# Performance work log

Hardware: AMD Instinct MI355X
Metric: run time of the kernel (lower is better)

The kernel has to match this reference:

```python
import jax, jax.numpy as jnp
import numpy as np

N = 6144          # num utterances (graph nodes)
D = 128           # utt_embed_size
WIN = 10          # att_window_size
NUM_SPK = 8
N_EMO = 7


def _init(key, shape):
    fan_in = shape[0]
    return jax.random.normal(key, shape, dtype=jnp.float32) * (1.0 / np.sqrt(fan_in))


def setup_inputs() -> dict:
    key = jax.random.key(0)
    ks = jax.random.split(key, 20)
    inp = {
        "x": jax.random.normal(ks[0], (N, D), dtype=jnp.float32),
        "speakers": jax.random.randint(ks[1], (N,), 0, NUM_SPK, dtype=jnp.int32),
        # layer-1 relation GCN weights (pred / suc / same / diff)
        "W_pred1": _init(ks[2], (D, D)),
        "W_suc1": _init(ks[3], (D, D)),
        "W_same1": _init(ks[4], (D, D)),
        "W_diff1": _init(ks[5], (D, D)),
        # layer-2 relation GCN weights
        "W_pred2": _init(ks[6], (D, D)),
        "W_suc2": _init(ks[7], (D, D)),
        "W_same2": _init(ks[8], (D, D)),
        "W_diff2": _init(ks[9], (D, D)),
        "w_aggr_1": _init(ks[10], (D, D)),
        "w_aggr_2": _init(ks[11], (D, D)),
        "w_e1": _init(ks[12], (2 * D, D)),
        "b_e1": jnp.zeros((D,), dtype=jnp.float32),
        "w_e2": _init(ks[13], (D, N_EMO)),
        "b_e2": jnp.zeros((N_EMO,), dtype=jnp.float32),
        "w_s": _init(ks[14], (2 * D, N_EMO)),
        "b_s": jnp.zeros((N_EMO,), dtype=jnp.float32),
    }
    return inp


def reference(x, speakers, W_pred1, W_suc1, W_same1, W_diff1,
              W_pred2, W_suc2, W_same2, W_diff2,
              w_aggr_1, w_aggr_2, w_e1, b_e1, w_e2, b_e2, w_s, b_s):
    n = x.shape[0]
    idx = jnp.arange(n)
    # windowed dot-product attention; entries outside the window stay 0.0
    # BEFORE the softmax (faithful to the torch code: zeros, not -inf)
    band = jnp.abs(idx[:, None] - idx[None, :]) <= WIN
    scores = jnp.where(band, x @ x.T, 0.0)            # [N, N]
    attn = jax.nn.softmax(scores, axis=1)
    # relation masks
    same = (speakers[:, None] == speakers[None, :]).astype(x.dtype)
    pred = (idx[None, :] >= idx[:, None]).astype(x.dtype)   # triu incl diag
    suc = 1.0 - pred                                          # strict lower tri
    adjs = (same * pred * attn,        # same-speaker, predecessor
            same * suc * attn,         # same-speaker, successor
            (1.0 - same) * pred * attn,  # diff-speaker, predecessor
            (1.0 - same) * suc * attn)   # diff-speaker, successor

    def gcn(h, Ws):  # sum_k adj_k @ (h @ W_k)
        return sum(a @ (h @ w) for a, w in zip(adjs, Ws))

    d = jnp.diagonal(attn)[:, None]   # self-attention scale
    h1 = jax.nn.relu(gcn(x, (W_pred1, W_suc1, W_same1, W_diff1))
                     + (x @ w_aggr_1) * d)
    h2 = jax.nn.relu(gcn(h1, (W_pred2, W_suc2, W_same2, W_diff2))
                     + (h1 @ w_aggr_2) * d)
    h = jnp.concatenate([h2, x], axis=1)              # [N, 2D]
    emotion = jax.nn.relu(h @ w_e1 + b_e1) @ w_e2 + b_e2   # [N, 7]
    sentiment = h @ w_s + b_s                               # [N, 7]
    return emotion, sentiment
```

## Files before the change

kernel.cpp:

```cpp
#include <hip/hip_runtime.h>
#include <hip/hip_bf16.h>


#define NN   6144
#define DD   128
#define WINW 10
#define YST  88

typedef unsigned short u16;
typedef __attribute__((ext_vector_type(8))) short bf16x8;
typedef __attribute__((ext_vector_type(4))) float f32x4;

__device__ __forceinline__ float b2f(u16 u) {
    return __uint_as_float(((unsigned int)u) << 16);
}
__device__ __forceinline__ u16 f2b(float f) {
    __hip_bfloat16 h = __float2bfloat16(f);
    return *reinterpret_cast<u16*>(&h);
}
__device__ __forceinline__ bf16x8 cvt8(const float* p) {
    float4 u = *reinterpret_cast<const float4*>(p);
    float4 v = *reinterpret_cast<const float4*>(p + 4);
    bf16x8 r;
    r[0] = (short)f2b(u.x); r[1] = (short)f2b(u.y);
    r[2] = (short)f2b(u.z); r[3] = (short)f2b(u.w);
    r[4] = (short)f2b(v.x); r[5] = (short)f2b(v.y);
    r[6] = (short)f2b(v.z); r[7] = (short)f2b(v.w);
    return r;
}

__global__ __launch_bounds__(256) void prep_kernel(
    const float* __restrict__ x,
    const float* __restrict__ p0, const float* __restrict__ p1,
    const float* __restrict__ p2, const float* __restrict__ p3,
    const float* __restrict__ p4,
    const float* __restrict__ q0, const float* __restrict__ q1,
    const float* __restrict__ q2, const float* __restrict__ q3,
    const float* __restrict__ q4,
    const float* __restrict__ we1, const float* __restrict__ we2,
    const float* __restrict__ ws,
    u16* __restrict__ W1T, u16* __restrict__ W2T, u16* __restrict__ We1T,
    u16* __restrict__ we2T, u16* __restrict__ wsT,
    float* __restrict__ bandw)
{
    const int tid = threadIdx.x;

    if (blockIdx.x < 64) {
        int t = blockIdx.x * 256 + tid;
        const float* Ws1[5] = {p0, p1, p2, p3, p4};
        const float* Ws2[5] = {q0, q1, q2, q3, q4};
        #pragma unroll
        for (int r = 0; r < 5; ++r) {
            int idx = t + r * 16384;
            int k = idx & 127, c = (idx >> 7) & 127;
            W1T[idx] = f2b(Ws1[r][k * 128 + c]);
            W2T[idx] = f2b(Ws2[r][k * 128 + c]);
        }
        #pragma unroll
        for (int r = 0; r < 2; ++r) {
            int idx = t + r * 16384;
            int n = idx >> 8, k = idx & 255;
            We1T[idx] = f2b(we1[k * 128 + n]);
        }
        if (blockIdx.x == 0) {
            #pragma unroll
            for (int r = 0; r < 8; ++r) {
                int idx = tid + r * 256;
                int n = idx >> 7, k = idx & 127;
                we2T[idx] = f2b(n < 7 ? we2[k * 7 + n] : 0.f);
            }
            #pragma unroll
            for (int r = 0; r < 16; ++r) {
                int idx = tid + r * 256;
                int n = idx >> 8, k = idx & 255;
                wsT[idx] = f2b(n < 7 ? ws[k * 7 + n] : 0.f);
            }
        }
        return;
    }

    __shared__ float Xs[52][132];
    __shared__ float Ss[32][24];
    const int r0 = (blockIdx.x - 64) * 32;

    #pragma unroll
    for (int it = 0; it < 7; ++it) {
        int f = tid + it * 256;
        if (f < 52 * 32) {
            int s = f >> 5, c = f & 31;
            int g = r0 - WINW + s;
            if (g >= 0 && g < NN)
                *reinterpret_cast<float4*>(&Xs[s][c * 4]) =
                    *reinterpret_cast<const float4*>(&x[(size_t)g * DD + c * 4]);
        }
    }
    __syncthreads();

    #pragma unroll
    for (int r = 0; r < 3; ++r) {
        int p = tid + r * 256;
        if (p >= 672) break;
        int il = p / 21, o = p - il * 21;
        int jg = r0 + il - WINW + o;
        float sv = -1e30f;
        if (jg >= 0 && jg < NN) {
            const float* xr = &Xs[il + WINW][0];
            const float* jr = &Xs[il + o][0];
            float a0 = 0.f, a1 = 0.f, a2 = 0.f, a3 = 0.f;
            #pragma unroll 8
            for (int k4 = 0; k4 < 32; ++k4) {
                float4 a = *reinterpret_cast<const float4*>(xr + k4 * 4);
                float4 b = *reinterpret_cast<const float4*>(jr + k4 * 4);
                a0 = fmaf(a.x, b.x, a0); a1 = fmaf(a.y, b.y, a1);
                a2 = fmaf(a.z, b.z, a2); a3 = fmaf(a.w, b.w, a3);
            }
            sv = (a0 + a1) + (a2 + a3);
        }
        Ss[il][o] = sv;
    }
    __syncthreads();

    if (tid < 32) {
        int il = tid, i = r0 + il;
        float m = 0.f;
        #pragma unroll
        for (int o = 0; o < 21; ++o) {
            float s = Ss[il][o];
            if (s > -1e29f) m = fmaxf(m, s);
        }
        int lo = i - WINW; if (lo < 0) lo = 0;
        int hi = i + WINW; if (hi > NN - 1) hi = NN - 1;
        float Z = (float)(NN - (hi - lo + 1)) * expf(-m);
        float ev[21];
        #pragma unroll
        for (int o = 0; o < 21; ++o) {
            float s = Ss[il][o];
            ev[o] = (s > -1e29f) ? expf(s - m) : 0.f;
            Z += ev[o];
        }
        #pragma unroll
        for (int o = 0; o < 21; ++o) bandw[i * 32 + o] = ev[o] / Z;
    }
}

__global__ __launch_bounds__(256, 4) void layer_kernel(
    const float* __restrict__ Af, const u16* __restrict__ Ab16,
    const u16* __restrict__ BT, const float* __restrict__ bandw,
    const int* __restrict__ spk, u16* __restrict__ hout, int a_is_f32)
{
    __shared__ u16 Ys[52][YST];
    __shared__ int2 tab[32 * 22];
    const int tid  = threadIdx.x;
    const int wave = tid >> 6, lane = tid & 63;
    const int lm = lane & 15, quad = lane >> 4;
    const int wm = wave >> 1, wn = wave & 1;
    const int bm = blockIdx.y * 32;
    const int hb = blockIdx.x;

    for (int p = tid; p < 704; p += 256) {
        int il = p / 22, e = p - il * 22;
        int i  = bm + il;
        int si = spk[i];
        float w; int off;
        if (e < 21) {
            int j = i - WINW + e;
            bool valid = (j >= 0) && (j < NN);
            int jc  = valid ? j : i;
            int sel = (spk[jc] == si) ? ((j >= i) ? 0 : 1) : ((j >= i) ? 2 : 3);
            w   = valid ? bandw[(size_t)i * 32 + e] : 0.f;
            off = valid ? (il + e) * YST + sel * 16 : 0;
        } else {
            w   = bandw[(size_t)i * 32 + WINW];
            off = (il + WINW) * YST + 4 * 16;
        }
        tab[p] = make_int2(__float_as_int(w), off);
    }

    bf16x8 afr[2][4];
    #pragma unroll
    for (int mt = 0; mt < 2; ++mt) {
        int gr = bm - WINW + (wm * 2 + mt) * 16 + lm;
        gr = min(max(gr, 0), NN - 1);
        #pragma unroll
        for (int s = 0; s < 4; ++s) {
            if (a_is_f32)
                afr[mt][s] = cvt8(Af + (size_t)gr * DD + s * 32 + quad * 8);
            else
                afr[mt][s] = *reinterpret_cast<const bf16x8*>(
                    Ab16 + (size_t)gr * DD + s * 32 + quad * 8);
        }
    }

    f32x4 acc[2][3];
    #pragma unroll
    for (int mt = 0; mt < 2; ++mt)
        #pragma unroll
        for (int n = 0; n < 3; ++n) acc[mt][n] = {0.f, 0.f, 0.f, 0.f};

    #pragma unroll
    for (int np = 0; np < 3; ++np) {
        int nt = wn * 3 + np;
        if (nt < 5) {
            int gn = nt * 128 + hb * 16 + lm;
            #pragma unroll
            for (int s = 0; s < 4; ++s) {
                bf16x8 b = *reinterpret_cast<const bf16x8*>(
                    BT + (size_t)gn * DD + s * 32 + quad * 8);
                acc[0][np] = __builtin_amdgcn_mfma_f32_16x16x32_bf16(afr[0][s], b, acc[0][np], 0, 0, 0);
                acc[1][np] = __builtin_amdgcn_mfma_f32_16x16x32_bf16(afr[1][s], b, acc[1][np], 0, 0, 0);
            }
        }
    }
    #pragma unroll
    for (int mt = 0; mt < 2; ++mt)
        #pragma unroll
        for (int np = 0; np < 3; ++np) {
            int nt = wn * 3 + np;
            if (nt < 5) {
                #pragma unroll
                for (int r = 0; r < 4; ++r) {
                    int lr = (wm * 2 + mt) * 16 + quad * 4 + r;
                    if (lr < 52) Ys[lr][nt * 16 + lm] = f2b(acc[mt][np][r]);
                }
            }
        }
    __syncthreads();

    const int c0 = (tid & 7) * 2;
    const int il = tid >> 3;
    {
        float a0 = 0.f, a1 = 0.f;
        const int2* tp = &tab[il * 22];
        #pragma unroll
        for (int e = 0; e < 22; ++e) {
            int2 t = tp[e];
            float w = __int_as_float(t.x);
            unsigned y2 = *reinterpret_cast<const unsigned*>(
                &Ys[0][0] + t.y + c0);
            a0 = fmaf(w, b2f((u16)(y2 & 0xffff)), a0);
            a1 = fmaf(w, b2f((u16)(y2 >> 16)), a1);
        }
        int i = bm + il;
        unsigned pk = ((unsigned)f2b(fmaxf(a1, 0.f)) << 16) | f2b(fmaxf(a0, 0.f));
        *reinterpret_cast<unsigned*>(&hout[(size_t)i * DD + hb * 16 + c0]) = pk;
    }
}

__global__ __launch_bounds__(256) void head_kernel(
    const u16* __restrict__ h2b, const float* __restrict__ x,
    const u16* __restrict__ We1T, const float* __restrict__ be1,
    const u16* __restrict__ we2T, const float* __restrict__ be2,
    const u16* __restrict__ wsT,  const float* __restrict__ bs,
    float* __restrict__ out)
{
    __shared__ float Es[16][132];
    const int tid  = threadIdx.x;
    const int wave = tid >> 6, lane = tid & 63;
    const int lm = lane & 15, quad = lane >> 4;
    const int bm = blockIdx.x * 16;
    const int row = bm + lm;

    bf16x8 afr[8];
    #pragma unroll
    for (int s = 0; s < 4; ++s)
        afr[s] = *reinterpret_cast<const bf16x8*>(
            &h2b[(size_t)row * DD + s * 32 + quad * 8]);
    #pragma unroll
    for (int s = 4; s < 8; ++s)
        afr[s] = cvt8(&x[(size_t)row * DD + (s - 4) * 32 + quad * 8]);

    f32x4 accE[2], accS = {0.f, 0.f, 0.f, 0.f};
    #pragma unroll
    for (int n = 0; n < 2; ++n) accE[n] = {0.f, 0.f, 0.f, 0.f};

    #pragma unroll
    for (int s = 0; s < 8; ++s) {
        #pragma unroll
        for (int n = 0; n < 2; ++n) {
            int nt = wave * 2 + n;
            bf16x8 b = *reinterpret_cast<const bf16x8*>(
                &We1T[(size_t)(nt * 16 + lm) * 256 + s * 32 + quad * 8]);
            accE[n] = __builtin_amdgcn_mfma_f32_16x16x32_bf16(afr[s], b, accE[n], 0, 0, 0);
        }
        if (wave == 0) {
            bf16x8 bsf = *reinterpret_cast<const bf16x8*>(
                &wsT[(size_t)lm * 256 + s * 32 + quad * 8]);
            accS = __builtin_amdgcn_mfma_f32_16x16x32_bf16(afr[s], bsf, accS, 0, 0, 0);
        }
    }

    if (wave == 0 && lm < 7) {
        #pragma unroll
        for (int r = 0; r < 4; ++r) {
            int i = bm + quad * 4 + r;
            out[(size_t)NN * 7 + (size_t)i * 7 + lm] = accS[r] + bs[lm];
        }
    }
    #pragma unroll
    for (int n = 0; n < 2; ++n) {
        int col = (wave * 2 + n) * 16 + lm;
        float bias = be1[col];
        #pragma unroll
        for (int r = 0; r < 4; ++r)
            Es[quad * 4 + r][col] = fmaxf(accE[n][r] + bias, 0.f);
    }
    __syncthreads();

    if (wave == 0) {
        f32x4 accM = {0.f, 0.f, 0.f, 0.f};
        #pragma unroll
        for (int s = 0; s < 4; ++s) {
            bf16x8 a = cvt8(&Es[lm][s * 32 + quad * 8]);
            bf16x8 b = *reinterpret_cast<const bf16x8*>(
                &we2T[(size_t)lm * 128 + s * 32 + quad * 8]);
            accM = __builtin_amdgcn_mfma_f32_16x16x32_bf16(a, b, accM, 0, 0, 0);
        }
        if (lm < 7) {
            #pragma unroll
            for (int r = 0; r < 4; ++r) {
                int i = bm + quad * 4 + r;
                out[(size_t)i * 7 + lm] = accM[r] + be2[lm];
            }
        }
    }
}

extern "C" void kernel_launch(void* const* d_in, const int* in_sizes, int n_in,
                              void* d_out, int out_size, void* d_ws, size_t ws_size,
                              hipStream_t stream)
{
    const float* x   = (const float*)d_in[0];
    const int*   spk = (const int*)d_in[1];
    const float* Wp1 = (const float*)d_in[2];
    const float* Wu1 = (const float*)d_in[3];
    const float* Wm1 = (const float*)d_in[4];
    const float* Wd1 = (const float*)d_in[5];
    const float* Wp2 = (const float*)d_in[6];
    const float* Wu2 = (const float*)d_in[7];
    const float* Wm2 = (const float*)d_in[8];
    const float* Wd2 = (const float*)d_in[9];
    const float* wa1 = (const float*)d_in[10];
    const float* wa2 = (const float*)d_in[11];
    const float* we1 = (const float*)d_in[12];
    const float* be1 = (const float*)d_in[13];
    const float* we2 = (const float*)d_in[14];
    const float* be2 = (const float*)d_in[15];
    const float* wss = (const float*)d_in[16];
    const float* bss = (const float*)d_in[17];

    char* base = (char*)d_ws;
    float* bandw = (float*)(base);
    u16*   W1T   = (u16*)(base + 786432);
    u16*   W2T   = (u16*)(base + 950272);
    u16*   We1T  = (u16*)(base + 1114112);
    u16*   we2T  = (u16*)(base + 1179648);
    u16*   wsT   = (u16*)(base + 1183744);
    u16*   h1b   = (u16*)(base + 1191936);
    u16*   h2b   = (u16*)(base + 2764800);

    prep_kernel<<<256, 256, 0, stream>>>(x, Wp1, Wu1, Wm1, Wd1, wa1,
                                         Wp2, Wu2, Wm2, Wd2, wa2,
                                         we1, we2, wss,
                                         W1T, W2T, We1T, we2T, wsT, bandw);
    layer_kernel<<<dim3(8, 192), 256, 0, stream>>>(x, nullptr, W1T, bandw, spk, h1b, 1);
    layer_kernel<<<dim3(8, 192), 256, 0, stream>>>(nullptr, h1b, W2T, bandw, spk, h2b, 0);
    head_kernel<<<384, 256, 0, stream>>>(h2b, x, We1T, be1, we2T, be2, wsT, bss,
                                         (float*)d_out);
}
```

Measured before the change: 153.6 us.

## Fuse prep, both GCN layers and head into one persistent kernel with grid barriers

Replaces the four kernel launches with one persistent kernel of 768 blocks that synchronizes stages through atomic-counter grid barriers in workspace, reset by a memset. The layer tiles are widened so each block produces 32 output columns instead of 16, giving a 4x192 tile grid that matches the persistent block count, and the attention prep is split across more blocks of 16 rows. This removes launch gaps and inter-kernel drain between stages. The barrier depends on all 768 blocks being co-resident, and the spin wait and atomics add latency.

```diff
diff --git a/kernel.cpp b/kernel.cpp
--- a/kernel.cpp
+++ b/kernel.cpp
@@ -5,7 +5,11 @@
 #define NN   6144
 #define DD   128
 #define WINW 10
-#define YST  88
+#define YST  168
+#define TAB_OFF 20544
+#define SM_BYTES 26176
+#define NBLK 768
+#define BAR_OFF 4337664
 
 typedef unsigned short u16;
 typedef __attribute__((ext_vector_type(8))) short bf16x8;
@@ -29,24 +33,150 @@
     return r;
 }
 
-__global__ __launch_bounds__(256) void prep_kernel(
-    const float* __restrict__ x,
+__device__ __forceinline__ void grid_barrier(unsigned* ctr) {
+    __threadfence();
+    __syncthreads();
+    if (threadIdx.x == 0) {
+        __hip_atomic_fetch_add(ctr, 1u, __ATOMIC_RELEASE,
+                               __HIP_MEMORY_SCOPE_AGENT);
+        while (__hip_atomic_load(ctr, __ATOMIC_RELAXED,
+                                 __HIP_MEMORY_SCOPE_AGENT) < (unsigned)NBLK)
+            __builtin_amdgcn_s_sleep(2);
+    }
+    __syncthreads();
+    __threadfence();
+}
+
+__device__ __forceinline__ void layer_tile(
+    const float* __restrict__ Af, const u16* __restrict__ Ab16,
+    const u16* __restrict__ BT, const float* __restrict__ bandw,
+    const int* __restrict__ spk, u16* __restrict__ hout,
+    int a_is_f32, int build_tab, int hb, int bm, char* smraw, int tid)
+{
+    u16*  Ys  = (u16*)smraw;
+    int2* tab = (int2*)(smraw + TAB_OFF);
+    const int wave = tid >> 6, lane = tid & 63;
+    const int lm = lane & 15, quad = lane >> 4;
+    const int wm = wave >> 1, wn = wave & 1;
+
+    if (build_tab) {
+        for (int p = tid; p < 704; p += 256) {
+            int il = p / 22, e = p - il * 22;
+            int i  = bm + il;
+            int si = spk[i];
+            float w; int off;
+            if (e < 21) {
+                int j = i - WINW + e;
+                bool valid = (j >= 0) && (j < NN);
+                int jc  = valid ? j : i;
+                int sel = (spk[jc] == si) ? ((j >= i) ? 0 : 1)
+                                          : ((j >= i) ? 2 : 3);
+                w   = valid ? bandw[(size_t)i * 32 + e] : 0.f;
+                off = valid ? (il + e) * YST + sel * 32 : 0;
+            } else {
+                w   = bandw[(size_t)i * 32 + WINW];
+                off = (il + WINW) * YST + 4 * 32;
+            }
+            tab[p] = make_int2(__float_as_int(w), off);
+        }
+    }
+
+    bf16x8 afr[2][4];
+    #pragma unroll
+    for (int mt = 0; mt < 2; ++mt) {
+        int gr = bm - WINW + (wm * 2 + mt) * 16 + lm;
+        gr = min(max(gr, 0), NN - 1);
+        #pragma unroll
+        for (int s = 0; s < 4; ++s) {
+            if (a_is_f32)
+                afr[mt][s] = cvt8(Af + (size_t)gr * DD + s * 32 + quad * 8);
+            else
+                afr[mt][s] = *reinterpret_cast<const bf16x8*>(
+                    Ab16 + (size_t)gr * DD + s * 32 + quad * 8);
+        }
+    }
+
+    f32x4 acc[2][5];
+    #pragma unroll
+    for (int mt = 0; mt < 2; ++mt)
+        #pragma unroll
+        for (int n = 0; n < 5; ++n) acc[mt][n] = {0.f, 0.f, 0.f, 0.f};
+
+    #pragma unroll
+    for (int np = 0; np < 5; ++np) {
+        int nt = wn * 5 + np;
+        int gn = (nt >> 1) * 128 + hb * 32 + (nt & 1) * 16 + lm;
+        #pragma unroll
+        for (int s = 0; s < 4; ++s) {
+            bf16x8 b = *reinterpret_cast<const bf16x8*>(
+                BT + (size_t)gn * DD + s * 32 + quad * 8);
+            acc[0][np] = __builtin_amdgcn_mfma_f32_16x16x32_bf16(afr[0][s], b, acc[0][np], 0, 0, 0);
+            acc[1][np] = __builtin_amdgcn_mfma_f32_16x16x32_bf16(afr[1][s], b, acc[1][np], 0, 0, 0);
+        }
+    }
+    #pragma unroll
+    for (int mt = 0; mt < 2; ++mt)
+        #pragma unroll
+        for (int np = 0; np < 5; ++np) {
+            int nt = wn * 5 + np;
+            #pragma unroll
+            for (int r = 0; r < 4; ++r) {
+                int lr = (wm * 2 + mt) * 16 + quad * 4 + r;
+                if (lr < 52) Ys[lr * YST + nt * 16 + lm] = f2b(acc[mt][np][r]);
+            }
+        }
+    __syncthreads();
+
+    const int c0 = (tid & 15) * 2;
+    const int rg = tid >> 4;
+    #pragma unroll
+    for (int rr = 0; rr < 2; ++rr) {
+        int il = rg * 2 + rr;
+        float a0 = 0.f, a1 = 0.f;
+        const int2* tp = &tab[il * 22];
+        #pragma unroll
+        for (int e = 0; e < 22; ++e) {
+            int2 t = tp[e];
+            float w = __int_as_float(t.x);
+            unsigned y2 = *reinterpret_cast<const unsigned*>(Ys + t.y + c0);
+            a0 = fmaf(w, b2f((u16)(y2 & 0xffff)), a0);
+            a1 = fmaf(w, b2f((u16)(y2 >> 16)), a1);
+        }
+        int i = bm + il;
+        unsigned pk = ((unsigned)f2b(fmaxf(a1, 0.f)) << 16) | f2b(fmaxf(a0, 0.f));
+        *reinterpret_cast<unsigned*>(&hout[(size_t)i * DD + hb * 32 + c0]) = pk;
+    }
+}
+
+__global__ __launch_bounds__(256, 4) void fused_kernel(
+    const float* __restrict__ x, const int* __restrict__ spk,
     const float* __restrict__ p0, const float* __restrict__ p1,
     const float* __restrict__ p2, const float* __restrict__ p3,
     const float* __restrict__ p4,
     const float* __restrict__ q0, const float* __restrict__ q1,
     const float* __restrict__ q2, const float* __restrict__ q3,
     const float* __restrict__ q4,
-    const float* __restrict__ we1, const float* __restrict__ we2,
-    const float* __restrict__ ws,
-    u16* __restrict__ W1T, u16* __restrict__ W2T, u16* __restrict__ We1T,
-    u16* __restrict__ we2T, u16* __restrict__ wsT,
-    float* __restrict__ bandw)
+    const float* __restrict__ we1, const float* __restrict__ be1,
+    const float* __restrict__ we2, const float* __restrict__ be2,
+    const float* __restrict__ wss, const float* __restrict__ bss,
+    float* __restrict__ out, char* __restrict__ ws)
 {
+    float* bandw = (float*)(ws);
+    u16*   W1T   = (u16*)(ws + 786432);
+    u16*   W2T   = (u16*)(ws + 950272);
+    u16*   We1T  = (u16*)(ws + 1114112);
+    u16*   we2T  = (u16*)(ws + 1179648);
+    u16*   wsT   = (u16*)(ws + 1183744);
+    u16*   h1b   = (u16*)(ws + 1191936);
+    u16*   h2b   = (u16*)(ws + 2764800);
+    unsigned* bar = (unsigned*)(ws + BAR_OFF);
+
+    __shared__ __align__(16) char smraw[SM_BYTES];
+    const int bid = blockIdx.x;
     const int tid = threadIdx.x;
 
-    if (blockIdx.x < 64) {
-        int t = blockIdx.x * 256 + tid;
+    if (bid < 64) {
+        int t = bid * 256 + tid;
         const float* Ws1[5] = {p0, p1, p2, p3, p4};
         const float* Ws2[5] = {q0, q1, q2, q3, q4};
         #pragma unroll
@@ -62,7 +192,7 @@
             int n = idx >> 8, k = idx & 255;
             We1T[idx] = f2b(we1[k * 128 + n]);
         }
-        if (blockIdx.x == 0) {
+        if (bid == 0) {
             #pragma unroll
             for (int r = 0; r < 8; ++r) {
                 int idx = tid + r * 256;
@@ -73,253 +203,159 @@
             for (int r = 0; r < 16; ++r) {
                 int idx = tid + r * 256;
                 int n = idx >> 8, k = idx & 255;
-                wsT[idx] = f2b(n < 7 ? ws[k * 7 + n] : 0.f);
-            }
-        }
-        return;
-    }
-
-    __shared__ float Xs[52][132];
-    __shared__ float Ss[32][24];
-    const int r0 = (blockIdx.x - 64) * 32;
-
-    #pragma unroll
-    for (int it = 0; it < 7; ++it) {
-        int f = tid + it * 256;
-        if (f < 52 * 32) {
-            int s = f >> 5, c = f & 31;
-            int g = r0 - WINW + s;
-            if (g >= 0 && g < NN)
-                *reinterpret_cast<float4*>(&Xs[s][c * 4]) =
-                    *reinterpret_cast<const float4*>(&x[(size_t)g * DD + c * 4]);
-        }
-    }
-    __syncthreads();
-
-    #pragma unroll
-    for (int r = 0; r < 3; ++r) {
-        int p = tid + r * 256;
-        if (p >= 672) break;
-        int il = p / 21, o = p - il * 21;
-        int jg = r0 + il - WINW + o;
-        float sv = -1e30f;
-        if (jg >= 0 && jg < NN) {
-            const float* xr = &Xs[il + WINW][0];
-            const float* jr = &Xs[il + o][0];
-            float a0 = 0.f, a1 = 0.f, a2 = 0.f, a3 = 0.f;
-            #pragma unroll 8
-            for (int k4 = 0; k4 < 32; ++k4) {
-                float4 a = *reinterpret_cast<const float4*>(xr + k4 * 4);
-                float4 b = *reinterpret_cast<const float4*>(jr + k4 * 4);
-                a0 = fmaf(a.x, b.x, a0); a1 = fmaf(a.y, b.y, a1);
-                a2 = fmaf(a.z, b.z, a2); a3 = fmaf(a.w, b.w, a3);
-            }
-            sv = (a0 + a1) + (a2 + a3);
-        }
-        Ss[il][o] = sv;
-    }
-    __syncthreads();
-
-    if (tid < 32) {
-        int il = tid, i = r0 + il;
-        float m = 0.f;
-        #pragma unroll
-        for (int o = 0; o < 21; ++o) {
-            float s = Ss[il][o];
-            if (s > -1e29f) m = fmaxf(m, s);
-        }
-        int lo = i - WINW; if (lo < 0) lo = 0;
-        int hi = i + WINW; if (hi > NN - 1) hi = NN - 1;
-        float Z = (float)(NN - (hi - lo + 1)) * expf(-m);
-        float ev[21];
-        #pragma unroll
-        for (int o = 0; o < 21; ++o) {
-            float s = Ss[il][o];
-            ev[o] = (s > -1e29f) ? expf(s - m) : 0.f;
-            Z += ev[o];
-        }
-        #pragma unroll
-        for (int o = 0; o < 21; ++o) bandw[i * 32 + o] = ev[o] / Z;
-    }
-}
-
-__global__ __launch_bounds__(256, 4) void layer_kernel(
-    const float* __restrict__ Af, const u16* __restrict__ Ab16,
-    const u16* __restrict__ BT, const float* __restrict__ bandw,
-    const int* __restrict__ spk, u16* __restrict__ hout, int a_is_f32)
-{
-    __shared__ u16 Ys[52][YST];
-    __shared__ int2 tab[32 * 22];
-    const int tid  = threadIdx.x;
-    const int wave = tid >> 6, lane = tid & 63;
-    const int lm = lane & 15, quad = lane >> 4;
-    const int wm = wave >> 1, wn = wave & 1;
-    const int bm = blockIdx.y * 32;
-    const int hb = blockIdx.x;
-
-    for (int p = tid; p < 704; p += 256) {
-        int il = p / 22, e = p - il * 22;
-        int i  = bm + il;
-        int si = spk[i];
-        float w; int off;
-        if (e < 21) {
-            int j = i - WINW + e;
-            bool valid = (j >= 0) && (j < NN);
-            int jc  = valid ? j : i;
-            int sel = (spk[jc] == si) ? ((j >= i) ? 0 : 1) : ((j >= i) ? 2 : 3);
-            w   = valid ? bandw[(size_t)i * 32 + e] : 0.f;
-            off = valid ? (il + e) * YST + sel * 16 : 0;
-        } else {
-            w   = bandw[(size_t)i * 32 + WINW];
-            off = (il + WINW) * YST + 4 * 16;
-        }
-        tab[p] = make_int2(__float_as_int(w), off);
-    }
-
-    bf16x8 afr[2][4];
-    #pragma unroll
-    for (int mt = 0; mt < 2; ++mt) {
-        int gr = bm - WINW + (wm * 2 + mt) * 16 + lm;
-        gr = min(max(gr, 0), NN - 1);
-        #pragma unroll
-        for (int s = 0; s < 4; ++s) {
-            if (a_is_f32)
-                afr[mt][s] = cvt8(Af + (size_t)gr * DD + s * 32 + quad * 8);
-            else
-                afr[mt][s] = *reinterpret_cast<const bf16x8*>(
-                    Ab16 + (size_t)gr * DD + s * 32 + quad * 8);
-        }
-    }
-
-    f32x4 acc[2][3];
-    #pragma unroll
-    for (int mt = 0; mt < 2; ++mt)
-        #pragma unroll
-        for (int n = 0; n < 3; ++n) acc[mt][n] = {0.f, 0.f, 0.f, 0.f};
-
-    #pragma unroll
-    for (int np = 0; np < 3; ++np) {
-        int nt = wn * 3 + np;
-        if (nt < 5) {
-            int gn = nt * 128 + hb * 16 + lm;
+                wsT[idx] = f2b(n < 7 ? wss[k * 7 + n] : 0.f);
+            }
+        }
+    } else if (bid < 448) {
+        float* Xs = (float*)smraw;
+        float* Ss = (float*)(smraw + 36 * 132 * 4);
+        const int r0 = (bid - 64) * 16;
+
+        #pragma unroll
+        for (int it = 0; it < 5; ++it) {
+            int f = tid + it * 256;
+            if (f < 36 * 32) {
+                int s = f >> 5, c = f & 31;
+                int g = r0 - WINW + s;
+                if (g >= 0 && g < NN)
+                    *reinterpret_cast<float4*>(&Xs[s * 132 + c * 4]) =
+                        *reinterpret_cast<const float4*>(&x[(size_t)g * DD + c * 4]);
+            }
+        }
+        __syncthreads();
+
+        #pragma unroll
+        for (int r = 0; r < 2; ++r) {
+            int p = tid + r * 256;
+            if (p < 336) {
+                int il = p / 21, o = p - il * 21;
+                int jg = r0 + il - WINW + o;
+                float sv = -1e30f;
+                if (jg >= 0 && jg < NN) {
+                    const float* xr = &Xs[(il + WINW) * 132];
+                    const float* jr = &Xs[(il + o) * 132];
+                    float a0 = 0.f, a1 = 0.f, a2 = 0.f, a3 = 0.f;
+                    #pragma unroll 8
+                    for (int k4 = 0; k4 < 32; ++k4) {
+                        float4 a = *reinterpret_cast<const float4*>(xr + k4 * 4);
+                        float4 b = *reinterpret_cast<const float4*>(jr + k4 * 4);
+                        a0 = fmaf(a.x, b.x, a0); a1 = fmaf(a.y, b.y, a1);
+                        a2 = fmaf(a.z, b.z, a2); a3 = fmaf(a.w, b.w, a3);
+                    }
+                    sv = (a0 + a1) + (a2 + a3);
+                }
+                Ss[il * 24 + o] = sv;
+            }
+        }
+        __syncthreads();
+
+        if (tid < 16) {
+            int il = tid, i = r0 + il;
+            float m = 0.f;
+            #pragma unroll
+            for (int o = 0; o < 21; ++o) {
+                float s = Ss[il * 24 + o];
+                if (s > -1e29f) m = fmaxf(m, s);
+            }
+            int lo = i - WINW; if (lo < 0) lo = 0;
+            int hi = i + WINW; if (hi > NN - 1) hi = NN - 1;
+            float Z = (float)(NN - (hi - lo + 1)) * expf(-m);
+            float ev[21];
+            #pragma unroll
+            for (int o = 0; o < 21; ++o) {
+                float s = Ss[il * 24 + o];
+                ev[o] = (s > -1e29f) ? expf(s - m) : 0.f;
+                Z += ev[o];
+            }
+            #pragma unroll
+            for (int o = 0; o < 21; ++o) bandw[i * 32 + o] = ev[o] / Z;
+        }
+    }
+
+    grid_barrier(&bar[0]);
+
+    {
+        const int hb = bid & 3, bm = (bid >> 2) * 32;
+        layer_tile(x, nullptr, W1T, bandw, spk, h1b, 1, 1, hb, bm, smraw, tid);
+    }
+
+    grid_barrier(&bar[1]);
+
+    {
+        const int hb = bid & 3, bm = (bid >> 2) * 32;
+        layer_tile(nullptr, h1b, W2T, bandw, spk, h2b, 0, 0, hb, bm, smraw, tid);
+    }
+
+    grid_barrier(&bar[2]);
+
+    if (bid < 384) {
+        float* Es = (float*)smraw;
+        const int wave = tid >> 6, lane = tid & 63;
+        const int lm = lane & 15, quad = lane >> 4;
+        const int bm = bid * 16;
+        const int row = bm + lm;
+
+        bf16x8 afr[8];
+        #pragma unroll
+        for (int s = 0; s < 4; ++s)
+            afr[s] = *reinterpret_cast<const bf16x8*>(
+                &h2b[(size_t)row * DD + s * 32 + quad * 8]);
+        #pragma unroll
+        for (int s = 4; s < 8; ++s)
+            afr[s] = cvt8(&x[(size_t)row * DD + (s - 4) * 32 + quad * 8]);
+
+        f32x4 accE[2], accS = {0.f, 0.f, 0.f, 0.f};
+        #pragma unroll
+        for (int n = 0; n < 2; ++n) accE[n] = {0.f, 0.f, 0.f, 0.f};
+
+        #pragma unroll
+        for (int s = 0; s < 8; ++s) {
+            #pragma unroll
+            for (int n = 0; n < 2; ++n) {
+                int nt = wave * 2 + n;
+                bf16x8 b = *reinterpret_cast<const bf16x8*>(
+                    &We1T[(size_t)(nt * 16 + lm) * 256 + s * 32 + quad * 8]);
+                accE[n] = __builtin_amdgcn_mfma_f32_16x16x32_bf16(afr[s], b, accE[n], 0, 0, 0);
+            }
+            if (wave == 0) {
+                bf16x8 bsf = *reinterpret_cast<const bf16x8*>(
+                    &wsT[(size_t)lm * 256 + s * 32 + quad * 8]);
+                accS = __builtin_amdgcn_mfma_f32_16x16x32_bf16(afr[s], bsf, accS, 0, 0, 0);
+            }
+        }
+
+        if (wave == 0 && lm < 7) {
+            #pragma unroll
+            for (int r = 0; r < 4; ++r) {
+                int i = bm + quad * 4 + r;
+                out[(size_t)NN * 7 + (size_t)i * 7 + lm] = accS[r] + bss[lm];
+            }
+        }
+        #pragma unroll
+        for (int n = 0; n < 2; ++n) {
+            int col = (wave * 2 + n) * 16 + lm;
+            float bias = be1[col];
+            #pragma unroll
+            for (int r = 0; r < 4; ++r)
+                Es[(quad * 4 + r) * 132 + col] = fmaxf(accE[n][r] + bias, 0.f);
+        }
+        __syncthreads();
+
+        if (wave == 0) {
+            f32x4 accM = {0.f, 0.f, 0.f, 0.f};
             #pragma unroll
             for (int s = 0; s < 4; ++s) {
+                bf16x8 a = cvt8(&Es[lm * 132 + s * 32 + quad * 8]);
                 bf16x8 b = *reinterpret_cast<const bf16x8*>(
-                    BT + (size_t)gn * DD + s * 32 + quad * 8);
-                acc[0][np] = __builtin_amdgcn_mfma_f32_16x16x32_bf16(afr[0][s], b, acc[0][np], 0, 0, 0);
-                acc[1][np] = __builtin_amdgcn_mfma_f32_16x16x32_bf16(afr[1][s], b, acc[1][np], 0, 0, 0);
-            }
-        }
-    }
-    #pragma unroll
-    for (int mt = 0; mt < 2; ++mt)
-        #pragma unroll
-        for (int np = 0; np < 3; ++np) {
-            int nt = wn * 3 + np;
-            if (nt < 5) {
+                    &we2T[(size_t)lm * 128 + s * 32 + quad * 8]);
+                accM = __builtin_amdgcn_mfma_f32_16x16x32_bf16(a, b, accM, 0, 0, 0);
+            }
+            if (lm < 7) {
                 #pragma unroll
                 for (int r = 0; r < 4; ++r) {
-                    int lr = (wm * 2 + mt) * 16 + quad * 4 + r;
-                    if (lr < 52) Ys[lr][nt * 16 + lm] = f2b(acc[mt][np][r]);
+                    int i = bm + quad * 4 + r;
+                    out[(size_t)i * 7 + lm] = accM[r] + be2[lm];
                 }
-            }
-        }
-    __syncthreads();
-
-    const int c0 = (tid & 7) * 2;
-    const int il = tid >> 3;
-    {
-        float a0 = 0.f, a1 = 0.f;
-        const int2* tp = &tab[il * 22];
-        #pragma unroll
-        for (int e = 0; e < 22; ++e) {
-            int2 t = tp[e];
-            float w = __int_as_float(t.x);
-            unsigned y2 = *reinterpret_cast<const unsigned*>(
-                &Ys[0][0] + t.y + c0);
-            a0 = fmaf(w, b2f((u16)(y2 & 0xffff)), a0);
-            a1 = fmaf(w, b2f((u16)(y2 >> 16)), a1);
-        }
-        int i = bm + il;
-        unsigned pk = ((unsigned)f2b(fmaxf(a1, 0.f)) << 16) | f2b(fmaxf(a0, 0.f));
-        *reinterpret_cast<unsigned*>(&hout[(size_t)i * DD + hb * 16 + c0]) = pk;
-    }
-}
-
-__global__ __launch_bounds__(256) void head_kernel(
-    const u16* __restrict__ h2b, const float* __restrict__ x,
-    const u16* __restrict__ We1T, const float* __restrict__ be1,
-    const u16* __restrict__ we2T, const float* __restrict__ be2,
-    const u16* __restrict__ wsT,  const float* __restrict__ bs,
-    float* __restrict__ out)
-{
-    __shared__ float Es[16][132];
-    const int tid  = threadIdx.x;
-    const int wave = tid >> 6, lane = tid & 63;
-    const int lm = lane & 15, quad = lane >> 4;
-    const int bm = blockIdx.x * 16;
-    const int row = bm + lm;
-
-    bf16x8 afr[8];
-    #pragma unroll
-    for (int s = 0; s < 4; ++s)
-        afr[s] = *reinterpret_cast<const bf16x8*>(
-            &h2b[(size_t)row * DD + s * 32 + quad * 8]);
-    #pragma unroll
-    for (int s = 4; s < 8; ++s)
-        afr[s] = cvt8(&x[(size_t)row * DD + (s - 4) * 32 + quad * 8]);
-
-    f32x4 accE[2], accS = {0.f, 0.f, 0.f, 0.f};
-    #pragma unroll
-    for (int n = 0; n < 2; ++n) accE[n] = {0.f, 0.f, 0.f, 0.f};
-
-    #pragma unroll
-    for (int s = 0; s < 8; ++s) {
-        #pragma unroll
-        for (int n = 0; n < 2; ++n) {
-            int nt = wave * 2 + n;
-            bf16x8 b = *reinterpret_cast<const bf16x8*>(
-                &We1T[(size_t)(nt * 16 + lm) * 256 + s * 32 + quad * 8]);
-            accE[n] = __builtin_amdgcn_mfma_f32_16x16x32_bf16(afr[s], b, accE[n], 0, 0, 0);
-        }
-        if (wave == 0) {
-            bf16x8 bsf = *reinterpret_cast<const bf16x8*>(
-                &wsT[(size_t)lm * 256 + s * 32 + quad * 8]);
-            accS = __builtin_amdgcn_mfma_f32_16x16x32_bf16(afr[s], bsf, accS, 0, 0, 0);
-        }
-    }
-
-    if (wave == 0 && lm < 7) {
-        #pragma unroll
-        for (int r = 0; r < 4; ++r) {
-            int i = bm + quad * 4 + r;
-            out[(size_t)NN * 7 + (size_t)i * 7 + lm] = accS[r] + bs[lm];
-        }
-    }
-    #pragma unroll
-    for (int n = 0; n < 2; ++n) {
-        int col = (wave * 2 + n) * 16 + lm;
-        float bias = be1[col];
-        #pragma unroll
-        for (int r = 0; r < 4; ++r)
-            Es[quad * 4 + r][col] = fmaxf(accE[n][r] + bias, 0.f);
-    }
-    __syncthreads();
-
-    if (wave == 0) {
-        f32x4 accM = {0.f, 0.f, 0.f, 0.f};
-        #pragma unroll
-        for (int s = 0; s < 4; ++s) {
-            bf16x8 a = cvt8(&Es[lm][s * 32 + quad * 8]);
-            bf16x8 b = *reinterpret_cast<const bf16x8*>(
-                &we2T[(size_t)lm * 128 + s * 32 + quad * 8]);
-            accM = __builtin_amdgcn_mfma_f32_16x16x32_bf16(a, b, accM, 0, 0, 0);
-        }
-        if (lm < 7) {
-            #pragma unroll
-            for (int r = 0; r < 4; ++r) {
-                int i = bm + quad * 4 + r;
-                out[(size_t)i * 7 + lm] = accM[r] + be2[lm];
             }
         }
     }
@@ -347,23 +383,12 @@
     const float* be2 = (const float*)d_in[15];
     const float* wss = (const float*)d_in[16];
     const float* bss = (const float*)d_in[17];
-
-    char* base = (char*)d_ws;
-    float* bandw = (float*)(base);
-    u16*   W1T   = (u16*)(base + 786432);
-    u16*   W2T   = (u16*)(base + 950272);
-    u16*   We1T  = (u16*)(base + 1114112);
-    u16*   we2T  = (u16*)(base + 1179648);
-    u16*   wsT   = (u16*)(base + 1183744);
-    u16*   h1b   = (u16*)(base + 1191936);
-    u16*   h2b   = (u16*)(base + 2764800);
-
-    prep_kernel<<<256, 256, 0, stream>>>(x, Wp1, Wu1, Wm1, Wd1, wa1,
-                                         Wp2, Wu2, Wm2, Wd2, wa2,
-                                         we1, we2, wss,
-                                         W1T, W2T, We1T, we2T, wsT, bandw);
-    layer_kernel<<<dim3(8, 192), 256, 0, stream>>>(x, nullptr, W1T, bandw, spk, h1b, 1);
-    layer_kernel<<<dim3(8, 192), 256, 0, stream>>>(nullptr, h1b, W2T, bandw, spk, h2b, 0);
-    head_kernel<<<384, 256, 0, stream>>>(h2b, x, We1T, be1, we2T, be2, wsT, bss,
-                                         (float*)d_out);
-}
+    float* out = (float*)d_out;
+    char*  ws  = (char*)d_ws;
+
+    hipMemsetAsync(ws + BAR_OFF, 0, 64, stream);
+
+    fused_kernel<<<dim3(NBLK), dim3(256), 0, stream>>>(
+        x, spk, Wp1, Wu1, Wm1, Wd1, wa1, Wp2, Wu2, Wm2, Wd2, wa2,
+        we1, be1, we2, be2, wss, bss, out, ws);
+}
```

Measured after the change: 576.7 us. 3.76x slower.
